# Kernel tuning notes

Hardware: AMD Instinct MI355X
Metric: run time of the kernel (lower is better)

Reference implementation:

```python
import jax, jax.numpy as jnp
import numpy as np

N_NODES = 100000


def gcn_layer(x, edge_index, W, b):
    """PyG GCNConv: h = D^-1/2 (A+I) D^-1/2 (x W) + b, scatter-sum aggregation."""
    n = x.shape[0]
    h = x @ W  # [N, out]
    loop = jnp.arange(n, dtype=edge_index.dtype)
    src = jnp.concatenate([edge_index[0], loop])  # [E+N]
    dst = jnp.concatenate([edge_index[1], loop])
    deg = jax.ops.segment_sum(jnp.ones_like(dst, dtype=h.dtype), dst, num_segments=n)
    dinv = jnp.where(deg > 0, jax.lax.rsqrt(deg), 0.0)
    norm = dinv[src] * dinv[dst]  # [E+N]
    msg = h[src] * norm[:, None]  # gather + scale (largest intermediate)
    out = jax.ops.segment_sum(msg, dst, num_segments=n)
    return out + b


def setup_inputs() -> dict:
    key = jax.random.key(0)
    k = jax.random.split(key, 8)
    in_dim, hid_dim, out_dim = 128, 64, 112
    E = 1600000
    x = jax.random.normal(k[0], (N_NODES, in_dim), dtype=jnp.float32)
    edge_index = jax.random.randint(k[1], (2, E), 0, N_NODES, dtype=jnp.int32)
    s1 = 1.0 / np.sqrt(in_dim)
    s2 = 1.0 / np.sqrt(hid_dim)
    return {
        "x": x,
        "edge_index": edge_index,
        "W1": jax.random.uniform(k[2], (in_dim, hid_dim), jnp.float32, -s1, s1),
        "b1": jnp.zeros((hid_dim,), jnp.float32),
        "W2": jax.random.uniform(k[3], (hid_dim, hid_dim), jnp.float32, -s2, s2),
        "b2": jnp.zeros((hid_dim,), jnp.float32),
        "W3": jax.random.uniform(k[4], (hid_dim, out_dim), jnp.float32, -s2, s2),
        "b3": jnp.zeros((out_dim,), jnp.float32),
    }


def reference(x, edge_index, W1, b1, W2, b2, W3, b3):
    # eval mode: dropout is identity
    h = jax.nn.relu(gcn_layer(x, edge_index, W1, b1))
    h = jax.nn.relu(gcn_layer(h, edge_index, W2, b2))
    return gcn_layer(h, edge_index, W3, b3)
```

## Files before the change

### kernel.cpp

```cpp
#include <hip/hip_runtime.h>
#include <hip/hip_fp16.h>
#include <math.h>


#define IN_DIM 128
#define HID 64
#define OUT_DIM 112
#define LSHIFT 7
#define LMASK 127
#define MAXBUCK 1024
#define CHUNK 8192
#define CAP 4096

typedef _Float16 f16x8 __attribute__((ext_vector_type(8)));
typedef float f32x4 __attribute__((ext_vector_type(4)));

template <int K, int C>
__device__ __forceinline__ void stage_w(const float* __restrict__ W, _Float16* Wt) {
  constexpr int KP = K + 8;
  for (int idx = threadIdx.x; idx < K * C; idx += 256) {
    int k = idx / C, c = idx % C;
    Wt[c * KP + k] = (_Float16)W[idx];
  }
}

template <int K, int C, bool XH, bool DINV, bool BIAS, bool OUTH>
__device__ __forceinline__ void gemm_compute(int blk, const void* __restrict__ Xv,
                                             const float* __restrict__ dinv,
                                             const float* __restrict__ bias,
                                             void* __restrict__ G, int n,
                                             const _Float16* Wt) {
  constexpr int KP = K + 8;
  constexpr int NT = C / 16;
  constexpr int KS = K / 32;
  const int tid = threadIdx.x;
  const int l = tid & 63;
  const int rbase = blk * 64 + (tid >> 6) * 16;
  const int kg = (l >> 4) * 8;
  const int c16 = l & 15;

  int arow = rbase + c16;
  if (arow >= n) arow = n - 1;
  f16x8 af[KS];
  if (XH) {
    const _Float16* Xh = reinterpret_cast<const _Float16*>(Xv);
#pragma unroll
    for (int ks = 0; ks < KS; ++ks)
      af[ks] = *reinterpret_cast<const f16x8*>(&Xh[(size_t)arow * K + ks * 32 + kg]);
  } else {
    const float* Xf = reinterpret_cast<const float*>(Xv);
#pragma unroll
    for (int ks = 0; ks < KS; ++ks) {
      float4 u0 = *reinterpret_cast<const float4*>(&Xf[(size_t)arow * K + ks * 32 + kg]);
      float4 u1 = *reinterpret_cast<const float4*>(&Xf[(size_t)arow * K + ks * 32 + kg + 4]);
      f16x8 a;
      a[0] = (_Float16)u0.x; a[1] = (_Float16)u0.y; a[2] = (_Float16)u0.z; a[3] = (_Float16)u0.w;
      a[4] = (_Float16)u1.x; a[5] = (_Float16)u1.y; a[6] = (_Float16)u1.z; a[7] = (_Float16)u1.w;
      af[ks] = a;
    }
  }

  f32x4 acc[NT];
#pragma unroll
  for (int nt = 0; nt < NT; ++nt) acc[nt] = (f32x4){0.f, 0.f, 0.f, 0.f};

#pragma unroll
  for (int ks = 0; ks < KS; ++ks) {
#pragma unroll
    for (int nt = 0; nt < NT; ++nt) {
      f16x8 bf = *reinterpret_cast<const f16x8*>(&Wt[(nt * 16 + c16) * KP + ks * 32 + kg]);
      acc[nt] = __builtin_amdgcn_mfma_f32_16x16x32_f16(af[ks], bf, acc[nt], 0, 0, 0);
    }
  }

#pragma unroll
  for (int r = 0; r < 4; ++r) {
    int grow = rbase + (l >> 4) * 4 + r;
    if (grow < n) {
      float s = DINV ? dinv[grow] : 1.0f;
#pragma unroll
      for (int nt = 0; nt < NT; ++nt) {
        float v = acc[nt][r] * s;
        if (BIAS) v += bias[nt * 16 + c16];
        if (OUTH)
          reinterpret_cast<__half*>(G)[(size_t)grow * C + nt * 16 + c16] = __float2half(v);
        else
          reinterpret_cast<float*>(G)[(size_t)grow * C + nt * 16 + c16] = v;
      }
    }
  }
}

template <int K, int C, bool XH, bool DINV, bool BIAS, bool OUTH>
__global__ __launch_bounds__(256) void mfma_gemm_kernel(const void* __restrict__ Xv,
                                                        const float* __restrict__ W,
                                                        const float* __restrict__ dinv,
                                                        const float* __restrict__ bias,
                                                        void* __restrict__ G, int n) {
  __shared__ _Float16 Wt[C * (K + 8)];
  stage_w<K, C>(W, Wt);
  __syncthreads();
  gemm_compute<K, C, XH, DINV, BIAS, OUTH>(blockIdx.x, Xv, dinv, bias, G, n, Wt);
}

__global__ __launch_bounds__(256) void gemm1_hist_kernel(
    const float* __restrict__ x, const float* __restrict__ W1, __half* __restrict__ gh,
    int n, const int* __restrict__ dst, int* __restrict__ H,
    int E, int nbuck, int nchunk) {
  __shared__ __align__(16) char smem[HID * (IN_DIM + 8) * 2];
  const int tid = threadIdx.x;
  if ((int)blockIdx.x < nchunk) {
    int* hist = reinterpret_cast<int*>(smem);
    for (int i = tid; i < nbuck; i += 256) hist[i] = 0;
    __syncthreads();
    int lo = blockIdx.x * CHUNK, hi = min(E, lo + CHUNK);
    for (int i = lo + tid; i < hi; i += 256)
      atomicAdd(&hist[dst[i] >> LSHIFT], 1);
    __syncthreads();
    int* Hrow = &H[(size_t)blockIdx.x * nbuck];
    for (int i = tid; i < nbuck; i += 256) Hrow[i] = hist[i];
  } else {
    _Float16* Wt = reinterpret_cast<_Float16*>(smem);
    stage_w<IN_DIM, HID>(W1, Wt);
    __syncthreads();
    gemm_compute<IN_DIM, HID, false, false, false, true>(
        (int)blockIdx.x - nchunk, x, nullptr, nullptr, gh, n, Wt);
  }
}

__global__ __launch_bounds__(256) void chunk_prefix_kernel(int* __restrict__ H,
                                                           int* __restrict__ cb,
                                                           int nchunk, int nbuck) {
  int wv = threadIdx.x >> 6, lane = threadIdx.x & 63;
  int b = blockIdx.x * 4 + wv;
  if (b >= nbuck) return;
  int run = 0;
  for (int c0 = 0; c0 < nchunk; c0 += 64) {
    int c = c0 + lane;
    int v = (c < nchunk) ? H[(size_t)c * nbuck + b] : 0;
    int incl = v;
#pragma unroll
    for (int off = 1; off < 64; off <<= 1) {
      int u = __shfl_up(incl, off);
      if (lane >= off) incl += u;
    }
    if (c < nchunk) H[(size_t)c * nbuck + b] = run + incl - v;
    run += __shfl(incl, 63);
  }
  if (lane == 0) cb[b] = run;
}

__global__ __launch_bounds__(256) void coarse_scatter_kernel(
    const int* __restrict__ src, const int* __restrict__ dst,
    const int* __restrict__ H, int* __restrict__ packed, int E, int nbuck) {
  __shared__ int cur[MAXBUCK];
  const int tid = threadIdx.x;
  const int* Hrow = &H[(size_t)blockIdx.x * nbuck];
  for (int i = tid; i < nbuck; i += 256) cur[i] = Hrow[i];
  __syncthreads();
  int lo = blockIdx.x * CHUNK, hi = min(E, lo + CHUNK);
  for (int i = lo + tid; i < hi; i += 256) {
    int s = src[i], d = dst[i];
    int b = d >> LSHIFT;
    int off = atomicAdd(&cur[b], 1);
    if (off < CAP) packed[(size_t)b * CAP + off] = (s << LSHIFT) | (d & LMASK);
  }
}

__global__ __launch_bounds__(256) void fine_fused_kernel(
    const int* __restrict__ packed, const int* __restrict__ cb,
    int* __restrict__ row_start, float* __restrict__ dinv,
    int* __restrict__ ssrc, __half* __restrict__ gh, int n, int nbuck) {
  const int b = blockIdx.x;
  const int t = threadIdx.x;
  __shared__ int hist[128];
  __shared__ int pfx[128];
  __shared__ int cur[128];
  __shared__ float sdi[128];
  __shared__ int red[4];
  __shared__ int sbase;
  if (t < 128) hist[t] = 0;
  __syncthreads();
  const int cbb = min(cb[b], CAP);
  const int* pk = &packed[(size_t)b * CAP];
  for (int e = t; e < cbb; e += 256) atomicAdd(&hist[pk[e] & LMASK], 1);
  int partial = 0;
  for (int i = t; i < b; i += 256) partial += min(cb[i], CAP);
#pragma unroll
  for (int off = 1; off < 64; off <<= 1) partial += __shfl_xor(partial, off);
  const int lane = t & 63, wv = t >> 6;
  if (lane == 0) red[wv] = partial;
  __syncthreads();
  if (t == 0) sbase = red[0] + red[1] + red[2] + red[3];
  if (t < 128) pfx[t] = hist[t];
  __syncthreads();
  for (int off = 1; off < 128; off <<= 1) {
    int u = (t >= off && t < 128) ? pfx[t - off] : 0;
    __syncthreads();
    if (t < 128) pfx[t] += u;
    __syncthreads();
  }
  if (t < 128) {
    int node = b * 128 + t;
    if (node < n) {
      int rs = sbase + pfx[t] - hist[t];
      row_start[node] = rs;
      float di = 1.0f / sqrtf((float)(hist[t] + 1));
      dinv[node] = di;
      sdi[t] = di;
      cur[t] = rs;
    } else {
      sdi[t] = 0.f;
      cur[t] = 0;
    }
  }
  if (b == nbuck - 1 && t == 0) row_start[n] = sbase + cbb;
  __syncthreads();
  for (int e = t; e < cbb; e += 256) {
    int p = pk[e];
    int slot = atomicAdd(&cur[p & LMASK], 1);
    ssrc[slot] = p >> LSHIFT;
  }
  __half2* g2 = reinterpret_cast<__half2*>(gh);
  for (int i = t; i < 128 * 32; i += 256) {
    int nd = i >> 5;
    int node = b * 128 + nd;
    if (node < n) {
      int q = i & 31;
      float2 f = __half22float2(g2[(size_t)node * 32 + q]);
      float d = sdi[nd];
      g2[(size_t)node * 32 + q] = __floats2half2_rn(f.x * d, f.y * d);
    }
  }
}

template <bool RELU, bool BIAS, bool TSCALE>
__global__ __launch_bounds__(256) void agg_kernel(const __half* __restrict__ g,
                                                  const int* __restrict__ row_start,
                                                  const int* __restrict__ ssrc,
                                                  const float* __restrict__ dinv,
                                                  const float* __restrict__ bias,
                                                  __half* __restrict__ out, int n) {
  const int tid = threadIdx.x;
  const int wv = tid >> 6;
  const int lane = tid & 63;
  const int h = lane >> 5;
  const int q = lane & 31;
  int node = blockIdx.x * 4 + wv;
  if (node >= n) return;
  const __half2* g2 = reinterpret_cast<const __half2*>(g);

  int e0 = row_start[node];
  int e1 = row_start[node + 1];
  int deg = e1 - e0;
  float2 acc = make_float2(0.f, 0.f);
  if (h == 0) {
    float2 sv = __half22float2(g2[(size_t)node * 32 + q]);
    acc.x = sv.x; acc.y = sv.y;
  }
  const int pairs = deg >> 1;
  const int base = e0 + h;
  int k = 0;
  for (; k + 8 <= pairs; k += 8) {
    int idx[8];
#pragma unroll
    for (int i = 0; i < 8; ++i) idx[i] = ssrc[base + 2 * (k + i)];
    __half2 v[8];
#pragma unroll
    for (int i = 0; i < 8; ++i) v[i] = g2[(size_t)idx[i] * 32 + q];
#pragma unroll
    for (int i = 0; i < 8; ++i) {
      float2 f = __half22float2(v[i]);
      acc.x += f.x; acc.y += f.y;
    }
  }
  for (; k + 2 <= pairs; k += 2) {
    int i0 = ssrc[base + 2 * k];
    int i1 = ssrc[base + 2 * (k + 1)];
    float2 f0 = __half22float2(g2[(size_t)i0 * 32 + q]);
    float2 f1 = __half22float2(g2[(size_t)i1 * 32 + q]);
    acc.x += f0.x + f1.x; acc.y += f0.y + f1.y;
  }
  for (; k < pairs; ++k) {
    int i0 = ssrc[base + 2 * k];
    float2 f = __half22float2(g2[(size_t)i0 * 32 + q]);
    acc.x += f.x; acc.y += f.y;
  }
  if ((deg & 1) && h == 0) {
    int i0 = ssrc[e1 - 1];
    float2 f = __half22float2(g2[(size_t)i0 * 32 + q]);
    acc.x += f.x; acc.y += f.y;
  }
  acc.x += __shfl_xor(acc.x, 32);
  acc.y += __shfl_xor(acc.y, 32);

  if (h == 0) {
    float di = dinv[node];
    float rx = acc.x * di, ry = acc.y * di;
    if (BIAS) {
      float2 bv = *reinterpret_cast<const float2*>(&bias[2 * q]);
      rx += bv.x; ry += bv.y;
    }
    if (RELU) { rx = fmaxf(rx, 0.f); ry = fmaxf(ry, 0.f); }
    if (TSCALE) { rx *= di; ry *= di; }
    reinterpret_cast<__half2*>(out)[(size_t)node * 32 + q] = __floats2half2_rn(rx, ry);
  }
}

extern "C" void kernel_launch(void* const* d_in, const int* in_sizes, int n_in,
                              void* d_out, int out_size, void* d_ws, size_t ws_size,
                              hipStream_t stream) {
  const float* x = (const float*)d_in[0];
  const int* ei = (const int*)d_in[1];
  const float* W1 = (const float*)d_in[2];
  const float* b1 = (const float*)d_in[3];
  const float* W2 = (const float*)d_in[4];
  const float* b2 = (const float*)d_in[5];
  const float* W3 = (const float*)d_in[6];
  const float* b3 = (const float*)d_in[7];
  float* out = (float*)d_out;

  const int n = in_sizes[0] / IN_DIM;
  const int E = in_sizes[1] / 2;
  const int* src = ei;
  const int* dst = ei + E;
  const int nbuck = (n + LMASK) >> LSHIFT;
  const int nchunk = (E + CHUNK - 1) / CHUNK;

  char* p = (char*)d_ws;
  auto alloc = [&](size_t bytes) {
    char* q = p;
    p += (bytes + 255) & ~(size_t)255;
    return q;
  };
  float* dinv = (float*)alloc((size_t)n * 4);
  int* row_start = (int*)alloc((size_t)(n + 1) * 4);
  int* H = (int*)alloc((size_t)nchunk * nbuck * 4);
  int* cb = (int*)alloc((size_t)(nbuck + 1) * 4);
  int* packed = (int*)alloc((size_t)nbuck * CAP * 4);
  int* ssrc = (int*)alloc((size_t)E * 4);
  __half* gh  = (__half*)alloc((size_t)n * HID * 2);
  __half* h1h = (__half*)alloc((size_t)n * HID * 2);
  __half* th  = (__half*)alloc((size_t)n * HID * 2);

  const int GG = (n + 63) / 64;
  const int AGRID = (n + 3) / 4;

  gemm1_hist_kernel<<<nchunk + GG, 256, 0, stream>>>(x, W1, gh, n, dst, H, E, nbuck, nchunk);
  chunk_prefix_kernel<<<(nbuck + 3) / 4, 256, 0, stream>>>(H, cb, nchunk, nbuck);
  coarse_scatter_kernel<<<nchunk, 256, 0, stream>>>(src, dst, H, packed, E, nbuck);
  fine_fused_kernel<<<nbuck, 256, 0, stream>>>(packed, cb, row_start, dinv, ssrc, gh, n, nbuck);

  agg_kernel<true, true, false><<<AGRID, 256, 0, stream>>>(gh, row_start, ssrc, dinv, b1, h1h, n);

  mfma_gemm_kernel<HID, HID, true, true, false, true><<<GG, 256, 0, stream>>>(h1h, W2, dinv, nullptr, gh, n);
  agg_kernel<true, true, true><<<AGRID, 256, 0, stream>>>(gh, row_start, ssrc, dinv, b2, th, n);

  agg_kernel<false, false, false><<<AGRID, 256, 0, stream>>>(th, row_start, ssrc, dinv, nullptr, h1h, n);
  mfma_gemm_kernel<HID, OUT_DIM, true, false, true, false><<<GG, 256, 0, stream>>>(h1h, W3, nullptr, b3, out, n);
}
```

Before: 352.6 us.

## Replace two-level bucketed CSR build with global-atomic counting sort

Swaps the chunked histogram, chunk prefix, coarse bucket scatter and fine per-bucket sort for a simpler CSR build. In-degrees are counted with global atomics per destination, a fused kernel scans them into row_start and also writes dinv and pre-scales gh, and a single scatter kernel places sources using global atomic cursors. This drops a kernel launch and the packed intermediate buffer, but relies on heavily contended global atomics over 100k nodes and gives a nondeterministic order of neighbours within each row. The scan kernel also re-reads all preceding counts in every block to get its base offset.

```diff
diff --git a/kernel.cpp b/kernel.cpp
--- a/kernel.cpp
+++ b/kernel.cpp
@@ -6,11 +6,8 @@
 #define IN_DIM 128
 #define HID 64
 #define OUT_DIM 112
-#define LSHIFT 7
-#define LMASK 127
-#define MAXBUCK 1024
-#define CHUNK 8192
-#define CAP 4096
+#define SCAN_TILE 1024
+#define NHIST 256
 
 typedef _Float16 f16x8 __attribute__((ext_vector_type(8)));
 typedef float f32x4 __attribute__((ext_vector_type(4)));
@@ -103,134 +100,103 @@
   gemm_compute<K, C, XH, DINV, BIAS, OUTH>(blockIdx.x, Xv, dinv, bias, G, n, Wt);
 }
 
-__global__ __launch_bounds__(256) void gemm1_hist_kernel(
+__global__ __launch_bounds__(256) void hist_gemm1_kernel(
     const float* __restrict__ x, const float* __restrict__ W1, __half* __restrict__ gh,
-    int n, const int* __restrict__ dst, int* __restrict__ H,
-    int E, int nbuck, int nchunk) {
-  __shared__ __align__(16) char smem[HID * (IN_DIM + 8) * 2];
+    int n, const int* __restrict__ dst, int* __restrict__ cnt, int E) {
+  __shared__ _Float16 Wt[HID * (IN_DIM + 8)];
   const int tid = threadIdx.x;
-  if ((int)blockIdx.x < nchunk) {
-    int* hist = reinterpret_cast<int*>(smem);
-    for (int i = tid; i < nbuck; i += 256) hist[i] = 0;
-    __syncthreads();
-    int lo = blockIdx.x * CHUNK, hi = min(E, lo + CHUNK);
-    for (int i = lo + tid; i < hi; i += 256)
-      atomicAdd(&hist[dst[i] >> LSHIFT], 1);
-    __syncthreads();
-    int* Hrow = &H[(size_t)blockIdx.x * nbuck];
-    for (int i = tid; i < nbuck; i += 256) Hrow[i] = hist[i];
+  if ((int)blockIdx.x < NHIST) {
+    for (int i = blockIdx.x * 256 + tid; i < E; i += NHIST * 256)
+      atomicAdd(&cnt[dst[i]], 1);
   } else {
-    _Float16* Wt = reinterpret_cast<_Float16*>(smem);
     stage_w<IN_DIM, HID>(W1, Wt);
     __syncthreads();
     gemm_compute<IN_DIM, HID, false, false, false, true>(
-        (int)blockIdx.x - nchunk, x, nullptr, nullptr, gh, n, Wt);
-  }
-}
-
-__global__ __launch_bounds__(256) void chunk_prefix_kernel(int* __restrict__ H,
-                                                           int* __restrict__ cb,
-                                                           int nchunk, int nbuck) {
-  int wv = threadIdx.x >> 6, lane = threadIdx.x & 63;
-  int b = blockIdx.x * 4 + wv;
-  if (b >= nbuck) return;
-  int run = 0;
-  for (int c0 = 0; c0 < nchunk; c0 += 64) {
-    int c = c0 + lane;
-    int v = (c < nchunk) ? H[(size_t)c * nbuck + b] : 0;
-    int incl = v;
-#pragma unroll
-    for (int off = 1; off < 64; off <<= 1) {
-      int u = __shfl_up(incl, off);
-      if (lane >= off) incl += u;
-    }
-    if (c < nchunk) H[(size_t)c * nbuck + b] = run + incl - v;
-    run += __shfl(incl, 63);
-  }
-  if (lane == 0) cb[b] = run;
-}
-
-__global__ __launch_bounds__(256) void coarse_scatter_kernel(
-    const int* __restrict__ src, const int* __restrict__ dst,
-    const int* __restrict__ H, int* __restrict__ packed, int E, int nbuck) {
-  __shared__ int cur[MAXBUCK];
-  const int tid = threadIdx.x;
-  const int* Hrow = &H[(size_t)blockIdx.x * nbuck];
-  for (int i = tid; i < nbuck; i += 256) cur[i] = Hrow[i];
-  __syncthreads();
-  int lo = blockIdx.x * CHUNK, hi = min(E, lo + CHUNK);
-  for (int i = lo + tid; i < hi; i += 256) {
-    int s = src[i], d = dst[i];
-    int b = d >> LSHIFT;
-    int off = atomicAdd(&cur[b], 1);
-    if (off < CAP) packed[(size_t)b * CAP + off] = (s << LSHIFT) | (d & LMASK);
-  }
-}
-
-__global__ __launch_bounds__(256) void fine_fused_kernel(
-    const int* __restrict__ packed, const int* __restrict__ cb,
-    int* __restrict__ row_start, float* __restrict__ dinv,
-    int* __restrict__ ssrc, __half* __restrict__ gh, int n, int nbuck) {
-  const int b = blockIdx.x;
+        (int)blockIdx.x - NHIST, x, nullptr, nullptr, gh, n, Wt);
+  }
+}
+
+__global__ __launch_bounds__(256) void scan_fused_kernel(
+    const int* __restrict__ cnt, int* __restrict__ row_start, int* __restrict__ cur,
+    float* __restrict__ dinv, __half* __restrict__ gh, int n, int E) {
   const int t = threadIdx.x;
-  __shared__ int hist[128];
-  __shared__ int pfx[128];
-  __shared__ int cur[128];
-  __shared__ float sdi[128];
-  __shared__ int red[4];
-  __shared__ int sbase;
-  if (t < 128) hist[t] = 0;
-  __syncthreads();
-  const int cbb = min(cb[b], CAP);
-  const int* pk = &packed[(size_t)b * CAP];
-  for (int e = t; e < cbb; e += 256) atomicAdd(&hist[pk[e] & LMASK], 1);
+  const int base = blockIdx.x * SCAN_TILE;
+  __shared__ int wred[4];
+  __shared__ int sh[256];
+  __shared__ float sdi[SCAN_TILE];
+
   int partial = 0;
-  for (int i = t; i < b; i += 256) partial += min(cb[i], CAP);
+  for (int i = t; i < base; i += 256) partial += cnt[i];
 #pragma unroll
   for (int off = 1; off < 64; off <<= 1) partial += __shfl_xor(partial, off);
   const int lane = t & 63, wv = t >> 6;
-  if (lane == 0) red[wv] = partial;
+  if (lane == 0) wred[wv] = partial;
+
+  const int i0 = base + t * 4;
+  int v0 = 0, v1 = 0, v2 = 0, v3 = 0;
+  if (i0 + 4 <= n) {
+    int4 v = *reinterpret_cast<const int4*>(&cnt[i0]);
+    v0 = v.x; v1 = v.y; v2 = v.z; v3 = v.w;
+  } else {
+    if (i0 + 0 < n) v0 = cnt[i0 + 0];
+    if (i0 + 1 < n) v1 = cnt[i0 + 1];
+    if (i0 + 2 < n) v2 = cnt[i0 + 2];
+    if (i0 + 3 < n) v3 = cnt[i0 + 3];
+  }
+  int s = v0 + v1 + v2 + v3;
+  sh[t] = s;
   __syncthreads();
-  if (t == 0) sbase = red[0] + red[1] + red[2] + red[3];
-  if (t < 128) pfx[t] = hist[t];
+  const int blockbase = wred[0] + wred[1] + wred[2] + wred[3];
+  for (int off = 1; off < 256; off <<= 1) {
+    int u = (t >= off) ? sh[t - off] : 0;
+    __syncthreads();
+    sh[t] += u;
+    __syncthreads();
+  }
+  int run = blockbase + sh[t] - s;
+  int p0 = run, p1 = run + v0, p2 = p1 + v1, p3 = p2 + v2;
+  if (i0 + 4 <= n) {
+    *reinterpret_cast<int4*>(&row_start[i0]) = make_int4(p0, p1, p2, p3);
+    *reinterpret_cast<int4*>(&cur[i0]) = make_int4(p0, p1, p2, p3);
+  } else {
+    if (i0 + 0 < n) { row_start[i0 + 0] = p0; cur[i0 + 0] = p0; }
+    if (i0 + 1 < n) { row_start[i0 + 1] = p1; cur[i0 + 1] = p1; }
+    if (i0 + 2 < n) { row_start[i0 + 2] = p2; cur[i0 + 2] = p2; }
+    if (i0 + 3 < n) { row_start[i0 + 3] = p3; cur[i0 + 3] = p3; }
+  }
+  float d0 = 1.0f / sqrtf((float)(v0 + 1));
+  float d1 = 1.0f / sqrtf((float)(v1 + 1));
+  float d2 = 1.0f / sqrtf((float)(v2 + 1));
+  float d3 = 1.0f / sqrtf((float)(v3 + 1));
+  if (i0 + 0 < n) dinv[i0 + 0] = d0;
+  if (i0 + 1 < n) dinv[i0 + 1] = d1;
+  if (i0 + 2 < n) dinv[i0 + 2] = d2;
+  if (i0 + 3 < n) dinv[i0 + 3] = d3;
+  sdi[t * 4 + 0] = d0; sdi[t * 4 + 1] = d1; sdi[t * 4 + 2] = d2; sdi[t * 4 + 3] = d3;
+  if (blockIdx.x == 0 && t == 0) row_start[n] = E;
   __syncthreads();
-  for (int off = 1; off < 128; off <<= 1) {
-    int u = (t >= off && t < 128) ? pfx[t - off] : 0;
-    __syncthreads();
-    if (t < 128) pfx[t] += u;
-    __syncthreads();
-  }
-  if (t < 128) {
-    int node = b * 128 + t;
-    if (node < n) {
-      int rs = sbase + pfx[t] - hist[t];
-      row_start[node] = rs;
-      float di = 1.0f / sqrtf((float)(hist[t] + 1));
-      dinv[node] = di;
-      sdi[t] = di;
-      cur[t] = rs;
-    } else {
-      sdi[t] = 0.f;
-      cur[t] = 0;
-    }
-  }
-  if (b == nbuck - 1 && t == 0) row_start[n] = sbase + cbb;
-  __syncthreads();
-  for (int e = t; e < cbb; e += 256) {
-    int p = pk[e];
-    int slot = atomicAdd(&cur[p & LMASK], 1);
-    ssrc[slot] = p >> LSHIFT;
-  }
   __half2* g2 = reinterpret_cast<__half2*>(gh);
-  for (int i = t; i < 128 * 32; i += 256) {
+  for (int i = t; i < SCAN_TILE * 32; i += 256) {
     int nd = i >> 5;
-    int node = b * 128 + nd;
+    int node = base + nd;
     if (node < n) {
       int q = i & 31;
       float2 f = __half22float2(g2[(size_t)node * 32 + q]);
       float d = sdi[nd];
       g2[(size_t)node * 32 + q] = __floats2half2_rn(f.x * d, f.y * d);
     }
+  }
+}
+
+__global__ __launch_bounds__(256) void scatter_kernel(const int* __restrict__ src,
+                                                      const int* __restrict__ dst,
+                                                      int* __restrict__ cur,
+                                                      int* __restrict__ ssrc, int E) {
+  const int stride = gridDim.x * 256;
+  for (int i = blockIdx.x * 256 + threadIdx.x; i < E; i += stride) {
+    int d = dst[i];
+    int pos = atomicAdd(&cur[d], 1);
+    ssrc[pos] = src[i];
   }
 }
 
@@ -324,8 +290,6 @@
   const int E = in_sizes[1] / 2;
   const int* src = ei;
   const int* dst = ei + E;
-  const int nbuck = (n + LMASK) >> LSHIFT;
-  const int nchunk = (E + CHUNK - 1) / CHUNK;
 
   char* p = (char*)d_ws;
   auto alloc = [&](size_t bytes) {
@@ -333,11 +297,10 @@
     p += (bytes + 255) & ~(size_t)255;
     return q;
   };
+  int* cnt = (int*)alloc((size_t)n * 4);
   float* dinv = (float*)alloc((size_t)n * 4);
   int* row_start = (int*)alloc((size_t)(n + 1) * 4);
-  int* H = (int*)alloc((size_t)nchunk * nbuck * 4);
-  int* cb = (int*)alloc((size_t)(nbuck + 1) * 4);
-  int* packed = (int*)alloc((size_t)nbuck * CAP * 4);
+  int* cur = (int*)alloc((size_t)n * 4);
   int* ssrc = (int*)alloc((size_t)E * 4);
   __half* gh  = (__half*)alloc((size_t)n * HID * 2);
   __half* h1h = (__half*)alloc((size_t)n * HID * 2);
@@ -345,11 +308,12 @@
 
   const int GG = (n + 63) / 64;
   const int AGRID = (n + 3) / 4;
-
-  gemm1_hist_kernel<<<nchunk + GG, 256, 0, stream>>>(x, W1, gh, n, dst, H, E, nbuck, nchunk);
-  chunk_prefix_kernel<<<(nbuck + 3) / 4, 256, 0, stream>>>(H, cb, nchunk, nbuck);
-  coarse_scatter_kernel<<<nchunk, 256, 0, stream>>>(src, dst, H, packed, E, nbuck);
-  fine_fused_kernel<<<nbuck, 256, 0, stream>>>(packed, cb, row_start, dinv, ssrc, gh, n, nbuck);
+  const int NB = (n + SCAN_TILE - 1) / SCAN_TILE;
+
+  hipMemsetAsync(cnt, 0, (size_t)n * 4, stream);
+  hist_gemm1_kernel<<<NHIST + GG, 256, 0, stream>>>(x, W1, gh, n, dst, cnt, E);
+  scan_fused_kernel<<<NB, 256, 0, stream>>>(cnt, row_start, cur, dinv, gh, n, E);
+  scatter_kernel<<<2048, 256, 0, stream>>>(src, dst, cur, ssrc, E);
 
   agg_kernel<true, true, false><<<AGRID, 256, 0, stream>>>(gh, row_start, ssrc, dinv, b1, h1h, n);
 
```

Result: slower. 545.6 us (+54.8%).
